# Performance work log

Measured on AMD Instinct MI355X. Metric: run time of the kernel, lower is better.

## Reference

```python
import jax, jax.numpy as jnp
import numpy as np

N, E, D_IN, LAT = 50000, 600000, 128, 64


def setup_inputs() -> dict:
    key = jax.random.key(0)
    ks = jax.random.split(key, 16)

    def w(k, i, o):
        return jax.random.normal(k, (i, o), jnp.float32) * (1.0 / np.sqrt(i))

    dims = [(D_IN, 64), (64, 128), (128, LAT)]
    inp = {
        "x": jax.random.normal(ks[0], (N, D_IN), jnp.float32),
        "edge_index": jax.random.randint(ks[1], (2, E), 0, N),
        "eps": jax.random.normal(ks[2], (N, LAT), jnp.float32),
    }
    for b_i, branch in enumerate(["mu", "ls"]):
        for li, (i, o) in enumerate(dims):
            inp[f"w_{branch}{li+1}"] = w(ks[3 + b_i * 3 + li], i, o)
            inp[f"b_{branch}{li+1}"] = jnp.zeros((o,), jnp.float32)
    return inp


def gcn(x, src, dst, dis, W, b):
    # GCNConv with add_self_loops=True and symmetric normalization:
    # out = D^-1/2 (A + I) D^-1/2 (x W) + b
    h = x @ W
    norm = dis[src] * dis[dst]                       # [E]
    agg = jax.ops.segment_sum(h[src] * norm[:, None], dst, num_segments=N)
    agg = agg + h * (dis * dis)[:, None]             # self-loop term d_i^-1 * h_i
    return agg + b


def encode_branch(x, src, dst, dis, ws, bs):
    h = x
    for W, b in zip(ws, bs):
        h = jax.nn.relu(gcn(h, src, dst, dis, W, b))  # ReLU after every GCNConv
    return h


def reference(x, edge_index, eps,
              w_mu1, b_mu1, w_mu2, b_mu2, w_mu3, b_mu3,
              w_ls1, b_ls1, w_ls2, b_ls2, w_ls3, b_ls3):
    src, dst = edge_index[0], edge_index[1]
    # degree with self loops (edge_weight = 1)
    deg = jax.ops.segment_sum(jnp.ones(E, x.dtype), dst, num_segments=N) + 1.0
    dis = jax.lax.rsqrt(deg)
    mu = encode_branch(x, src, dst, dis, [w_mu1, w_mu2, w_mu3], [b_mu1, b_mu2, b_mu3])
    logstd = encode_branch(x, src, dst, dis, [w_ls1, w_ls2, w_ls3], [b_ls1, b_ls2, b_ls3])
    logstd = jnp.minimum(logstd, 10.0)               # PyG VGAE MAX_LOGSTD clamp
    z = mu + eps * jnp.exp(logstd)                   # reparametrize (training=True)
    # VGAE inner-product decoder on observed edges, sigmoid=True
    adj = jax.nn.sigmoid(jnp.sum(z[src] * z[dst], axis=-1))
    return adj, mu, logstd
```

## Files before the change

### kernel.cpp

```cpp
#include <hip/hip_runtime.h>
#include <hip/hip_bf16.h>
#include <hip/hip_fp16.h>
#include <math.h>


typedef _Float16 hf2 __attribute__((ext_vector_type(2)));
static __device__ __forceinline__ hf2 as_hf2(unsigned u) {
    union { unsigned u; hf2 h; } c; c.u = u; return c.h;
}

__global__ void zero_int_k(int* __restrict__ p, int n) {
    int i = blockIdx.x * blockDim.x + threadIdx.x;
    if (i < n) p[i] = 0;
}

__global__ void count_dst_k(const int* __restrict__ ei, int* __restrict__ cnt, int E) {
    int e = blockIdx.x * blockDim.x + threadIdx.x;
    if (e < E) atomicAdd(&cnt[ei[E + e]], 1);
}

__global__ void compute_dis_k(const int* __restrict__ cnt, float* __restrict__ dis, int n) {
    int i = blockIdx.x * blockDim.x + threadIdx.x;
    if (i < n) dis[i] = rsqrtf((float)cnt[i] + 1.0f);
}

__global__ void scan1_k(const int* __restrict__ cnt, int* __restrict__ row_ptr,
                        int* __restrict__ bsum, int n) {
    __shared__ int wsum[16];
    int tid = threadIdx.x, lane = tid & 63, wv = tid >> 6;
    int i = blockIdx.x * 1024 + tid;
    int v = (i < n) ? cnt[i] : 0;
    int x = v;
#pragma unroll
    for (int off = 1; off < 64; off <<= 1) {
        int t = __shfl_up(x, off, 64);
        if (lane >= off) x += t;
    }
    if (lane == 63) wsum[wv] = x;
    __syncthreads();
    if (wv == 0 && lane < 16) {
        int y = wsum[lane];
#pragma unroll
        for (int off = 1; off < 16; off <<= 1) {
            int t = __shfl_up(y, off, 64);
            if (lane >= off) y += t;
        }
        wsum[lane] = y;
    }
    __syncthreads();
    int incl = x + ((wv == 0) ? 0 : wsum[wv - 1]);
    if (i < n) row_ptr[i + 1] = incl;
    if (tid == 1023) bsum[blockIdx.x] = incl;
}

__global__ void scan2_k(int* __restrict__ bsum, int nb) {
    int lane = threadIdx.x;
    int v = (lane < nb) ? bsum[lane] : 0;
    int x = v;
#pragma unroll
    for (int off = 1; off < 64; off <<= 1) {
        int t = __shfl_up(x, off, 64);
        if (lane >= off) x += t;
    }
    if (lane < nb) bsum[lane] = x - v;
}

__global__ void scan3_k(const int* __restrict__ cnt, int* __restrict__ row_ptr,
                        const int* __restrict__ bsum, int* __restrict__ woff, int n) {
    int i = blockIdx.x * 1024 + threadIdx.x;
    if (i == 0) row_ptr[0] = 0;
    if (i < n) {
        int r = row_ptr[i + 1] + bsum[blockIdx.x];
        row_ptr[i + 1] = r;
        woff[i] = r - cnt[i];
    }
}

__global__ void scatter_edges_k(const int* __restrict__ ei, int* __restrict__ woff,
                                int* __restrict__ src_sorted, int E) {
    int e = blockIdx.x * blockDim.x + threadIdx.x;
    if (e < E) {
        int s = ei[e];
        int d = ei[E + e];
        int pos = atomicAdd(&woff[d], 1);
        src_sorted[pos] = s;
    }
}

template <int K, int OUT, int EPI, int PRE, int AH>
__global__ __launch_bounds__(256, 4) void matmul2_k(
        const void* __restrict__ AAv, const void* __restrict__ ABv, int lda,
        int offaA, int offaB,
        const float* __restrict__ WA, const float* __restrict__ WB,
        const float* __restrict__ bA, const float* __restrict__ bB,
        __half* __restrict__ HHA, __half* __restrict__ HHB,
        const float* __restrict__ dis,
        int ldh, int offhA, int offhB, int n) {
    constexpr int TX = OUT / 4;
    constexpr int TY = 256 / TX;
    constexpr int TM = TY * 4;
    constexpr int KC = 32, KC4 = 8, KC8 = 4;
    __shared__ float w_lds[K * OUT];
    __shared__ float a_lds[TM * KC];

    int by = blockIdx.y;
    const float*  Af = (const float*)(by ? ABv : AAv);
    const __half* Ah = (const __half*)(by ? ABv : AAv);
    const float* W  = by ? WB : WA;
    const float* bi = by ? bB : bA;
    __half*      HH = by ? HHB : HHA;
    int offa = by ? offaB : offaA;
    int offh = by ? offhB : offhA;

    int tid = threadIdx.x;
    for (int idx = tid; idx < K * OUT / 4; idx += 256)
        ((float4*)w_lds)[idx] = ((const float4*)W)[idx];

    int row0 = blockIdx.x * TM;
    int tx = tid % TX;
    int ty = tid / TX;

    float4 acc[4];
#pragma unroll
    for (int i = 0; i < 4; ++i) acc[i] = make_float4(0.f, 0.f, 0.f, 0.f);

    int abase[4], akey[4];
#pragma unroll
    for (int i = 0; i < 4; ++i) {
        int r = ty * 4 + i;
        abase[i] = r * KC;
        akey[i]  = (r >> 2) & 7;
    }

    for (int kc = 0; kc < K; kc += KC) {
        __syncthreads();
        if constexpr (AH) {
            for (int f8 = tid; f8 < TM * KC8; f8 += 256) {
                int row  = f8 / KC8;
                int col8 = f8 % KC8;
                float f[8] = {0.f, 0.f, 0.f, 0.f, 0.f, 0.f, 0.f, 0.f};
                if (row0 + row < n) {
                    uint4 u = *(const uint4*)&Ah[(size_t)(row0 + row) * lda + offa + kc + col8 * 8];
                    const __half2* p = (const __half2*)&u;
#pragma unroll
                    for (int i = 0; i < 4; ++i) {
                        float2 t = __half22float2(p[i]);
                        f[2 * i] = t.x; f[2 * i + 1] = t.y;
                    }
                }
                int key = (row >> 2) & 7;
                *(float4*)&a_lds[row * KC + (((2 * col8) ^ key) << 2)] =
                    make_float4(f[0], f[1], f[2], f[3]);
                *(float4*)&a_lds[row * KC + (((2 * col8 + 1) ^ key) << 2)] =
                    make_float4(f[4], f[5], f[6], f[7]);
            }
        } else {
            for (int f4 = tid; f4 < TM * KC4; f4 += 256) {
                int row  = f4 >> 3;
                int col4 = f4 & 7;
                float4 v = make_float4(0.f, 0.f, 0.f, 0.f);
                if (row0 + row < n)
                    v = *(const float4*)&Af[(size_t)(row0 + row) * lda + offa + kc + (col4 << 2)];
                *(float4*)&a_lds[row * KC + ((col4 ^ ((row >> 2) & 7)) << 2)] = v;
            }
        }
        __syncthreads();

#pragma unroll
        for (int k = 0; k < KC; k += 4) {
            int k4 = k >> 2;
            float af[4][4];
#pragma unroll
            for (int i = 0; i < 4; ++i) {
                float4 a = *(const float4*)&a_lds[abase[i] + ((k4 ^ akey[i]) << 2)];
                af[i][0] = a.x; af[i][1] = a.y; af[i][2] = a.z; af[i][3] = a.w;
            }
#pragma unroll
            for (int j = 0; j < 4; ++j) {
                float4 wv = ((const float4*)w_lds)[(kc + k + j) * TX + tx];
#pragma unroll
                for (int i = 0; i < 4; ++i) {
                    acc[i].x += af[i][j] * wv.x;
                    acc[i].y += af[i][j] * wv.y;
                    acc[i].z += af[i][j] * wv.z;
                    acc[i].w += af[i][j] * wv.w;
                }
            }
        }
    }

#pragma unroll
    for (int i = 0; i < 4; ++i) {
        int r = row0 + ty * 4 + i;
        if (r < n) {
            float4 o = acc[i];
            if (EPI == 1) {
                float4 b = ((const float4*)bi)[tx];
                o.x = fmaxf(o.x + b.x, 0.f);
                o.y = fmaxf(o.y + b.y, 0.f);
                o.z = fmaxf(o.z + b.z, 0.f);
                o.w = fmaxf(o.w + b.w, 0.f);
            }
            float dsc = (PRE == 1) ? dis[r] : 1.f;
            __half2 h0 = __floats2half2_rn(o.x * dsc, o.y * dsc);
            __half2 h1 = __floats2half2_rn(o.z * dsc, o.w * dsc);
            uint2 u = make_uint2(*(unsigned*)&h0, *(unsigned*)&h1);
            *(uint2*)&HH[(size_t)r * ldh + offh + tx * 4] = u;
        }
    }
}

template <int MODE>
__global__ void agg2h_k(const __half* __restrict__ h, const float* __restrict__ dis,
                        const int* __restrict__ row_ptr, const int* __restrict__ srcs,
                        const float* __restrict__ bM, const float* __restrict__ bL,
                        const float* __restrict__ eps,
                        __half* __restrict__ oH,
                        float* __restrict__ oM, float* __restrict__ oL,
                        __half* __restrict__ zh, int n) {
    int wid  = (int)((blockIdx.x * (size_t)blockDim.x + threadIdx.x) >> 6);
    int lane = threadIdx.x & 63;
    if (wid >= n) return;
    int g = lane >> 4;
    int q = lane & 15;
    const __half* hq = h + 8 * q;

    __half2 acc2[4];
    if (g == 0) {
        uint4 r = *(const uint4*)&hq[(size_t)wid << 7];
        const __half2* hp = (const __half2*)&r;
#pragma unroll
        for (int i = 0; i < 4; ++i) acc2[i] = hp[i];
    } else {
        __half2 z2 = __float2half2_rn(0.f);
#pragma unroll
        for (int i = 0; i < 4; ++i) acc2[i] = z2;
    }

    int beg = row_ptr[wid], end = row_ptr[wid + 1];
    for (int cb = beg; cb < end; cb += 64) {
        int m = end - cb;
        if (m > 64) m = 64;
        int sv = 0;
        if (lane < m) sv = srcs[cb + lane];
        int j = 0;
        for (; j + 16 <= m; j += 16) {
            int s0 = __shfl(sv, j + g, 64);
            int s1 = __shfl(sv, j + 4 + g, 64);
            int s2 = __shfl(sv, j + 8 + g, 64);
            int s3 = __shfl(sv, j + 12 + g, 64);
            uint4 r0 = *(const uint4*)&hq[(size_t)s0 << 7];
            uint4 r1 = *(const uint4*)&hq[(size_t)s1 << 7];
            uint4 r2 = *(const uint4*)&hq[(size_t)s2 << 7];
            uint4 r3 = *(const uint4*)&hq[(size_t)s3 << 7];
            const __half2* p0 = (const __half2*)&r0;
            const __half2* p1 = (const __half2*)&r1;
            const __half2* p2 = (const __half2*)&r2;
            const __half2* p3 = (const __half2*)&r3;
#pragma unroll
            for (int i = 0; i < 4; ++i)
                acc2[i] = __hadd2(acc2[i],
                          __hadd2(__hadd2(p0[i], p1[i]), __hadd2(p2[i], p3[i])));
        }
        for (; j + 8 <= m; j += 8) {
            int s0 = __shfl(sv, j + g, 64);
            int s1 = __shfl(sv, j + 4 + g, 64);
            uint4 r0 = *(const uint4*)&hq[(size_t)s0 << 7];
            uint4 r1 = *(const uint4*)&hq[(size_t)s1 << 7];
            const __half2* p0 = (const __half2*)&r0;
            const __half2* p1 = (const __half2*)&r1;
#pragma unroll
            for (int i = 0; i < 4; ++i)
                acc2[i] = __hadd2(acc2[i], __hadd2(p0[i], p1[i]));
        }
        for (; j < m; j += 4) {
            int idx = j + g;
            int s0 = __shfl(sv, (idx < m) ? idx : j, 64);
            if (idx < m) {
                uint4 r0 = *(const uint4*)&hq[(size_t)s0 << 7];
                const __half2* p0 = (const __half2*)&r0;
#pragma unroll
                for (int i = 0; i < 4; ++i) acc2[i] = __hadd2(acc2[i], p0[i]);
            }
        }
    }

#pragma unroll
    for (int i = 0; i < 4; ++i) {
        int u0 = *reinterpret_cast<int*>(&acc2[i]);
        int v0 = __shfl_xor(u0, 16, 64);
        acc2[i] = __hadd2(acc2[i], *reinterpret_cast<__half2*>(&v0));
        int u1 = *reinterpret_cast<int*>(&acc2[i]);
        int v1 = __shfl_xor(u1, 32, 64);
        acc2[i] = __hadd2(acc2[i], *reinterpret_cast<__half2*>(&v1));
    }

    float di = dis[wid];
    float acc[8];
#pragma unroll
    for (int i = 0; i < 4; ++i) {
        float2 f = __half22float2(acc2[i]);
        acc[2 * i]     = f.x * di;
        acc[2 * i + 1] = f.y * di;
    }

    if (MODE == 0) {
        if (g == 0) {
            __half2 hh[4];
#pragma unroll
            for (int i = 0; i < 4; ++i) hh[i] = __floats2half2_rn(acc[2 * i], acc[2 * i + 1]);
            *(uint4*)&oH[(size_t)wid * 128 + 8 * q] = *(uint4*)hh;
        }
    } else if (MODE == 1) {
        if (g == 0) {
            const float* bs = (q < 8) ? bM + 8 * q : bL + 8 * q - 64;
            __half2 hh[4];
#pragma unroll
            for (int i = 0; i < 8; i += 2) {
                float a0 = fmaxf(acc[i] + bs[i], 0.f) * di;
                float a1 = fmaxf(acc[i + 1] + bs[i + 1], 0.f) * di;
                hh[i >> 1] = __floats2half2_rn(a0, a1);
            }
            *(uint4*)&oH[(size_t)wid * 128 + 8 * q] = *(uint4*)hh;
        }
    } else {
        const float* bs = (q < 8) ? bM + 8 * q : bL + 8 * q - 64;
        float act[8];
#pragma unroll
        for (int i = 0; i < 8; ++i) {
            float a = fmaxf(acc[i] + bs[i], 0.f);
            if (q >= 8) a = fminf(a, 10.f);
            act[i] = a;
        }
        float lsv[8];
#pragma unroll
        for (int i = 0; i < 8; ++i) lsv[i] = __shfl(act[i], lane + 8, 64);
        if (g == 0) {
            size_t ob = (size_t)wid * 64;
            if (q < 8) {
                *(float4*)&oM[ob + 8 * q]     = make_float4(act[0], act[1], act[2], act[3]);
                *(float4*)&oM[ob + 8 * q + 4] = make_float4(act[4], act[5], act[6], act[7]);
                float4 e0 = *(const float4*)&eps[ob + 8 * q];
                float4 e1 = *(const float4*)&eps[ob + 8 * q + 4];
                float zz[8];
                zz[0] = fmaf(e0.x, expf(lsv[0]), act[0]);
                zz[1] = fmaf(e0.y, expf(lsv[1]), act[1]);
                zz[2] = fmaf(e0.z, expf(lsv[2]), act[2]);
                zz[3] = fmaf(e0.w, expf(lsv[3]), act[3]);
                zz[4] = fmaf(e1.x, expf(lsv[4]), act[4]);
                zz[5] = fmaf(e1.y, expf(lsv[5]), act[5]);
                zz[6] = fmaf(e1.z, expf(lsv[6]), act[6]);
                zz[7] = fmaf(e1.w, expf(lsv[7]), act[7]);
                __half2 zh4[4];
#pragma unroll
                for (int i = 0; i < 4; ++i) zh4[i] = __floats2half2_rn(zz[2 * i], zz[2 * i + 1]);
                *(uint4*)&zh[ob + 8 * q] = *(uint4*)zh4;
            } else {
                int qq = q - 8;
                *(float4*)&oL[ob + 8 * qq]     = make_float4(act[0], act[1], act[2], act[3]);
                *(float4*)&oL[ob + 8 * qq + 4] = make_float4(act[4], act[5], act[6], act[7]);
            }
        }
    }
}

__global__ void decoder_k(const int* __restrict__ ei, const __half* __restrict__ zh,
                          float* __restrict__ adj, int E) {
    int t = blockIdx.x * 256 + threadIdx.x;
    int e = t >> 4;
    int q = threadIdx.x & 15;
    if (e >= E) return;
    int s = ei[e];
    int d = ei[E + e];
    const uint2* z2 = (const uint2*)zh;
    uint2 ua = z2[(size_t)s * 16 + q];
    uint2 ub = z2[(size_t)d * 16 + q];
    float p = 0.f;
#if defined(__has_builtin) && __has_builtin(__builtin_amdgcn_fdot2)
    p = __builtin_amdgcn_fdot2(as_hf2(ua.x), as_hf2(ub.x), p, false);
    p = __builtin_amdgcn_fdot2(as_hf2(ua.y), as_hf2(ub.y), p, false);
#else
    {
        const __half2* pa = (const __half2*)&ua;
        const __half2* pb = (const __half2*)&ub;
#pragma unroll
        for (int i = 0; i < 2; ++i) {
            float2 fa = __half22float2(pa[i]);
            float2 fb = __half22float2(pb[i]);
            p = fmaf(fa.x, fb.x, p);
            p = fmaf(fa.y, fb.y, p);
        }
    }
#endif
    p += __shfl_xor(p, 8);
    p += __shfl_xor(p, 4);
    p += __shfl_xor(p, 2);
    p += __shfl_xor(p, 1);
    if (q == 0) adj[e] = 1.f / (1.f + expf(-p));
}

extern "C" void kernel_launch(void* const* d_in, const int* in_sizes, int n_in,
                              void* d_out, int out_size, void* d_ws, size_t ws_size,
                              hipStream_t stream) {
    const float* x   = (const float*)d_in[0];
    const int*   ei  = (const int*)d_in[1];
    const float* eps = (const float*)d_in[2];
    const float* w_mu1 = (const float*)d_in[3];
    const float* b_mu1 = (const float*)d_in[4];
    const float* w_mu2 = (const float*)d_in[5];
    const float* b_mu2 = (const float*)d_in[6];
    const float* w_mu3 = (const float*)d_in[7];
    const float* b_mu3 = (const float*)d_in[8];
    const float* w_ls1 = (const float*)d_in[9];
    const float* b_ls1 = (const float*)d_in[10];
    const float* w_ls2 = (const float*)d_in[11];
    const float* b_ls2 = (const float*)d_in[12];
    const float* w_ls3 = (const float*)d_in[13];
    const float* b_ls3 = (const float*)d_in[14];

    const int N = in_sizes[0] / 128;
    const int E = in_sizes[1] / 2;
    const size_t NB = (size_t)N * 128;

    float* out = (float*)d_out;
    float* adj = out;
    float* mu  = out + E;
    float* ls  = out + E + (size_t)N * 64;

    float* ws = (float*)d_ws;
    __half* hpA  = (__half*)ws;
    __half* a2h  = (__half*)ws;
    __half* hpB  = (__half*)(ws + NB);
    __half* h2mu = (__half*)(ws + NB);
    __half* h2ls = h2mu + (size_t)N * 128;
    __half* zh   = (__half*)(ws + NB);
    float* c0 = ws + 2 * NB;
    const size_t P = 50176;
    float* dis         = c0;
    int*   cnt         = (int*)(c0 + P);
    int*   row_ptr     = (int*)(c0 + 2 * P);
    int*   woff        = (int*)(c0 + 3 * P);
    int*   bsum        = (int*)(c0 + 4 * P);
    int*   src_sorted  = (int*)(c0 + 4 * P + 256);

    const int nscan = (N + 1023) / 1024;

    zero_int_k<<<(N + 255) / 256, 256, 0, stream>>>(cnt, N);
    count_dst_k<<<(E + 255) / 256, 256, 0, stream>>>(ei, cnt, E);
    compute_dis_k<<<(N + 255) / 256, 256, 0, stream>>>(cnt, dis, N);
    scan1_k<<<nscan, 1024, 0, stream>>>(cnt, row_ptr, bsum, N);
    scan2_k<<<1, 64, 0, stream>>>(bsum, nscan);
    scan3_k<<<nscan, 1024, 0, stream>>>(cnt, row_ptr, bsum, woff, N);
    scatter_edges_k<<<(E + 255) / 256, 256, 0, stream>>>(ei, woff, src_sorted, E);

    const int aggBlocks = (int)(((size_t)N * 64 + 255) / 256);
    dim3 g64((N + 63) / 64, 2), g32((N + 31) / 32, 2);

    matmul2_k<128, 64, 0, 1, 0><<<g64, 256, 0, stream>>>(
        x, x, 128, 0, 0, w_mu1, w_ls1, nullptr, nullptr, hpA, hpA, dis, 128, 0, 64, N);
    agg2h_k<1><<<aggBlocks, 256, 0, stream>>>(hpA, dis, row_ptr, src_sorted,
                                              b_mu1, b_ls1, nullptr, hpB,
                                              nullptr, nullptr, nullptr, N);

    agg2h_k<0><<<aggBlocks, 256, 0, stream>>>(hpB, dis, row_ptr, src_sorted,
                                              nullptr, nullptr, nullptr, a2h,
                                              nullptr, nullptr, nullptr, N);
    matmul2_k<64, 128, 1, 0, 1><<<g32, 256, 0, stream>>>(
        a2h, a2h, 128, 0, 64, w_mu2, w_ls2, b_mu2, b_ls2, h2mu, h2ls, dis, 128, 0, 0, N);

    matmul2_k<128, 64, 0, 1, 1><<<g64, 256, 0, stream>>>(
        h2mu, h2ls, 128, 0, 0, w_mu3, w_ls3, nullptr, nullptr, hpA, hpA, dis, 128, 0, 64, N);
    agg2h_k<2><<<aggBlocks, 256, 0, stream>>>(hpA, dis, row_ptr, src_sorted,
                                              b_mu3, b_ls3, eps, nullptr,
                                              mu, ls, zh, N);

    decoder_k<<<(int)(((size_t)E * 16 + 255) / 256), 256, 0, stream>>>(ei, zh, adj, E);
}
```

Before: 272.3 us.

## Bin edges by destination bucket before CSR scatter; fuse dis into scan

Replaces the single random-scatter edge sort with a two-pass scheme. The first pass partitions edges into 256-node destination buckets using a shared-memory histogram and per-bucket global offsets. The second pass then scatters into CSR from the bucketed order, so its atomics and writes stay local in cache. The degree rsqrt is also folded into the first scan kernel, removing one launch. The cost is an extra pass over the edges plus an int2 intermediate buffer.

```diff
diff --git a/kernel.cpp b/kernel.cpp
--- a/kernel.cpp
+++ b/kernel.cpp
@@ -19,13 +19,8 @@
     if (e < E) atomicAdd(&cnt[ei[E + e]], 1);
 }
 
-__global__ void compute_dis_k(const int* __restrict__ cnt, float* __restrict__ dis, int n) {
-    int i = blockIdx.x * blockDim.x + threadIdx.x;
-    if (i < n) dis[i] = rsqrtf((float)cnt[i] + 1.0f);
-}
-
 __global__ void scan1_k(const int* __restrict__ cnt, int* __restrict__ row_ptr,
-                        int* __restrict__ bsum, int n) {
+                        int* __restrict__ bsum, float* __restrict__ dis, int n) {
     __shared__ int wsum[16];
     int tid = threadIdx.x, lane = tid & 63, wv = tid >> 6;
     int i = blockIdx.x * 1024 + tid;
@@ -49,7 +44,10 @@
     }
     __syncthreads();
     int incl = x + ((wv == 0) ? 0 : wsum[wv - 1]);
-    if (i < n) row_ptr[i + 1] = incl;
+    if (i < n) {
+        row_ptr[i + 1] = incl;
+        dis[i] = rsqrtf((float)v + 1.0f);
+    }
     if (tid == 1023) bsum[blockIdx.x] = incl;
 }
 
@@ -76,14 +74,43 @@
     }
 }
 
-__global__ void scatter_edges_k(const int* __restrict__ ei, int* __restrict__ woff,
-                                int* __restrict__ src_sorted, int E) {
-    int e = blockIdx.x * blockDim.x + threadIdx.x;
+__global__ __launch_bounds__(1024) void bin_edges_k(
+        const int* __restrict__ ei, const int* __restrict__ row_ptr,
+        int* __restrict__ bfill, int2* __restrict__ bin_sd, int E, int n) {
+    __shared__ int hist[256];
+    __shared__ int gbase[256];
+    int tid = threadIdx.x;
+    int nbuk = (n + 255) >> 8;
+    for (int b = tid; b < nbuk; b += 1024) hist[b] = 0;
+    __syncthreads();
+    int e = blockIdx.x * 1024 + tid;
+    int s = 0, d = 0, b = 0, lpos = 0;
+    bool val = (e < E);
+    if (val) {
+        s = ei[e];
+        d = ei[E + e];
+        b = d >> 8;
+        lpos = atomicAdd(&hist[b], 1);
+    }
+    __syncthreads();
+    for (int bb = tid; bb < nbuk; bb += 1024) {
+        int h = hist[bb];
+        gbase[bb] = h ? atomicAdd(&bfill[bb], h) : 0;
+    }
+    __syncthreads();
+    if (val) {
+        int base = row_ptr[b << 8];
+        bin_sd[base + gbase[b] + lpos] = make_int2(s, d);
+    }
+}
+
+__global__ void scatter2_k(const int2* __restrict__ bin_sd, int* __restrict__ woff,
+                           int* __restrict__ src_sorted, int E) {
+    int e = blockIdx.x * 256 + threadIdx.x;
     if (e < E) {
-        int s = ei[e];
-        int d = ei[E + e];
-        int pos = atomicAdd(&woff[d], 1);
-        src_sorted[pos] = s;
+        int2 sd = bin_sd[e];
+        int pos = atomicAdd(&woff[sd.y], 1);
+        src_sorted[pos] = sd.x;
     }
 }
 
@@ -435,23 +462,26 @@
     __half* h2ls = h2mu + (size_t)N * 128;
     __half* zh   = (__half*)(ws + NB);
     float* c0 = ws + 2 * NB;
-    const size_t P = 50176;
+    const size_t P  = 50176;
+    const size_t EP = 600064;
     float* dis         = c0;
     int*   cnt         = (int*)(c0 + P);
-    int*   row_ptr     = (int*)(c0 + 2 * P);
-    int*   woff        = (int*)(c0 + 3 * P);
-    int*   bsum        = (int*)(c0 + 4 * P);
-    int*   src_sorted  = (int*)(c0 + 4 * P + 256);
+    int*   bfill       = cnt + P;
+    int*   row_ptr     = (int*)(c0 + 2 * P + 256);
+    int*   woff        = (int*)(c0 + 3 * P + 256);
+    int*   bsum        = (int*)(c0 + 4 * P + 256);
+    int*   src_sorted  = (int*)(c0 + 4 * P + 512);
+    int2*  bin_sd      = (int2*)(c0 + 4 * P + 512 + EP);
 
     const int nscan = (N + 1023) / 1024;
 
-    zero_int_k<<<(N + 255) / 256, 256, 0, stream>>>(cnt, N);
+    zero_int_k<<<(int)((P + 256 + 255) / 256), 256, 0, stream>>>(cnt, (int)(P + 256));
     count_dst_k<<<(E + 255) / 256, 256, 0, stream>>>(ei, cnt, E);
-    compute_dis_k<<<(N + 255) / 256, 256, 0, stream>>>(cnt, dis, N);
-    scan1_k<<<nscan, 1024, 0, stream>>>(cnt, row_ptr, bsum, N);
+    scan1_k<<<nscan, 1024, 0, stream>>>(cnt, row_ptr, bsum, dis, N);
     scan2_k<<<1, 64, 0, stream>>>(bsum, nscan);
     scan3_k<<<nscan, 1024, 0, stream>>>(cnt, row_ptr, bsum, woff, N);
-    scatter_edges_k<<<(E + 255) / 256, 256, 0, stream>>>(ei, woff, src_sorted, E);
+    bin_edges_k<<<(E + 1023) / 1024, 1024, 0, stream>>>(ei, row_ptr, bfill, bin_sd, E, N);
+    scatter2_k<<<(E + 255) / 256, 256, 0, stream>>>(bin_sd, woff, src_sorted, E);
 
     const int aggBlocks = (int)(((size_t)N * 64 + 255) / 256);
     dim3 g64((N + 63) / 64, 2), g32((N + 31) / 32, 2);
```

New measurement: 272.3 us. Within noise of the previous version (-0.0%).
